# Optimization experiments

Measured on AMD Instinct MI355X. Metric: run time of the kernel, lower is better.

The kernel has to match this reference:

```python
import jax, jax.numpy as jnp
import numpy as np

N_NODES = 100000
N_EDGES = 3200000
N_GRAPHS = 64
IN_DIM = 4
HID = 64
EPS = 1e-5  # BatchNorm eps


def _batchnorm(x, gamma, beta):
    # training-mode batch norm over the node/graph axis (biased variance)
    mu = x.mean(axis=0)
    var = x.var(axis=0)
    return (x - mu) * jax.lax.rsqrt(var + EPS) * gamma + beta


def _gcn_conv(x, W, b, src, dst, n):
    # PyG GCNConv with add_self_loops=True, edge_weight=1:
    # out = D^{-1/2}(A+I)D^{-1/2} x W + b
    h = x @ W  # [N, out]
    deg = jax.ops.segment_sum(jnp.ones((src.shape[0],), h.dtype), dst,
                              num_segments=n) + 1.0  # +1 for self-loop
    dinv = jax.lax.rsqrt(deg)
    norm = dinv[src] * dinv[dst]  # [E]
    agg = jax.ops.segment_sum(h[src] * norm[:, None], dst, num_segments=n)
    # self-loop contribution: norm = 1/deg[i]
    return agg + h * (1.0 / deg)[:, None] + b


def setup_inputs() -> dict:
    key = jax.random.key(0)
    ks = jax.random.split(key, 12)
    s = 0.1
    inp = {
        "x": jax.random.normal(ks[0], (N_NODES, IN_DIM), jnp.float32),
        "edge_index": jax.random.randint(ks[1], (2, N_EDGES), 0, N_NODES, dtype=jnp.int64),
        "batch": jnp.sort(jax.random.randint(ks[2], (N_NODES,), 0, N_GRAPHS, dtype=jnp.int64)),
        # BatchNorm(4)
        "bn0_g": jnp.ones((IN_DIM,), jnp.float32),
        "bn0_b": jnp.zeros((IN_DIM,), jnp.float32),
        # GCNConv(4, 64)
        "W0": jax.random.normal(ks[3], (IN_DIM, HID), jnp.float32) * s,
        "b0": jnp.zeros((HID,), jnp.float32),
        # GCNConv(64, 64)
        "W1": jax.random.normal(ks[4], (HID, HID), jnp.float32) * s,
        "b1": jnp.zeros((HID,), jnp.float32),
        # BatchNorm(64) after pooling
        "bn1_g": jnp.ones((HID,), jnp.float32),
        "bn1_b": jnp.zeros((HID,), jnp.float32),
        # two hidden Linear(64, 64)
        "lin0_W": jax.random.normal(ks[5], (HID, HID), jnp.float32) * s,
        "lin0_b": jnp.zeros((HID,), jnp.float32),
        "lin1_W": jax.random.normal(ks[6], (HID, HID), jnp.float32) * s,
        "lin1_b": jnp.zeros((HID,), jnp.float32),
        # Linear(64, 1)
        "out_W": jax.random.normal(ks[7], (HID, 1), jnp.float32) * s,
        "out_b": jnp.zeros((1,), jnp.float32),
    }
    return inp


def reference(x, edge_index, batch, bn0_g, bn0_b, W0, b0, W1, b1,
              bn1_g, bn1_b, lin0_W, lin0_b, lin1_W, lin1_b, out_W, out_b):
    src, dst = edge_index[0], edge_index[1]
    h = _batchnorm(x, bn0_g, bn0_b)
    h = _gcn_conv(h, W0, b0, src, dst, N_NODES)
    h = _gcn_conv(h, W1, b1, src, dst, N_NODES)
    g = jax.ops.segment_sum(h, batch, num_segments=N_GRAPHS)  # global_add_pool
    g = _batchnorm(g, bn1_g, bn1_b)
    g = g @ lin0_W + lin0_b
    g = g @ lin1_W + lin1_b
    return g @ out_W + out_b  # [N_GRAPHS, 1]
```

## Files before the change

kernel.cpp:

```cpp
#include <hip/hip_runtime.h>
#include <hip/hip_bf16.h>

#define EPSF 1e-5f

static constexpr int NGRAPH = 64;
static constexpr int HBA = 512;
static constexpr int SH = 9;
static constexpr int GB = 256;
static constexpr int NBLK = 512;
static constexpr int BNB = 64;

__global__ __launch_bounds__(256) void k_pre(const float4* __restrict__ x,
                                             int N, const int* __restrict__ ei,
                                             int E, int chunk,
                                             float* __restrict__ bnpart,
                                             unsigned* __restrict__ counts) {
  __shared__ unsigned cnt[256];
  __shared__ float red[4][8];
  int t = threadIdx.x;
  if (blockIdx.x < BNB) {
    float s[4] = {0, 0, 0, 0}, q[4] = {0, 0, 0, 0};
    for (int i = blockIdx.x * 256 + t; i < N; i += BNB * 256) {
      float4 v = x[i];
      s[0] += v.x; q[0] += v.x * v.x;
      s[1] += v.y; q[1] += v.y * v.y;
      s[2] += v.z; q[2] += v.z * v.z;
      s[3] += v.w; q[3] += v.w * v.w;
    }
#pragma unroll
    for (int o = 32; o > 0; o >>= 1) {
#pragma unroll
      for (int k = 0; k < 4; k++) {
        s[k] += __shfl_down(s[k], o);
        q[k] += __shfl_down(q[k], o);
      }
    }
    int w = t >> 6;
    if ((t & 63) == 0) {
#pragma unroll
      for (int k = 0; k < 4; k++) {
        red[w][k] = s[k];
        red[w][4 + k] = q[k];
      }
    }
    __syncthreads();
    if (t < 8) {
      float a = red[0][t] + red[1][t] + red[2][t] + red[3][t];
      bnpart[blockIdx.x * 8 + t] = a;
    }
  } else {
    int g = blockIdx.x - BNB;
    cnt[t] = 0;
    __syncthreads();
    int lo = g * chunk, hi = min(E, lo + chunk);
    for (int base = lo + 4 * t; base < hi; base += 4 * 256) {
      int nv = min(4, hi - base);
      int d[4];
#pragma unroll
      for (int j = 0; j < 4; j++) d[j] = (j < nv) ? ei[E + base + j] : 0;
#pragma unroll
      for (int j = 0; j < 4; j++)
        if (j < nv) atomicAdd(&cnt[d[j] >> SH], 1u);
    }
    __syncthreads();
    counts[(size_t)g * 256 + t] = cnt[t];
  }
}

__global__ __launch_bounds__(1024) void k_boffA(
    const unsigned* __restrict__ counts, int E,
    const float* __restrict__ bnpart, unsigned* __restrict__ bucketStart,
    float* __restrict__ stats) {
  __shared__ unsigned tot4[1024];
  __shared__ unsigned tot[256];
  __shared__ unsigned scn[256];
  int tid = threadIdx.x;
  int b = tid & 255, q = tid >> 8;
  unsigned s = 0;
#pragma unroll 8
  for (int i = 0; i < 64; i++) s += counts[(size_t)(q * 64 + i) * 256 + b];
  tot4[tid] = s;
  if (tid < 8) {
    float a = 0.f;
#pragma unroll 8
    for (int i = 0; i < BNB; i++) a += bnpart[i * 8 + tid];
    stats[tid] = a;
  }
  __syncthreads();
  if (tid < 256) {
    unsigned v = tot4[tid] + tot4[256 + tid] + tot4[512 + tid] + tot4[768 + tid];
    tot[tid] = v;
    scn[tid] = v;
  }
  __syncthreads();
  for (int o = 1; o < 256; o <<= 1) {
    unsigned add = (tid < 256 && tid >= o) ? scn[tid - o] : 0u;
    __syncthreads();
    if (tid < 256) scn[tid] += add;
    __syncthreads();
  }
  if (tid < 256) bucketStart[tid] = scn[tid] - tot[tid];
  if (tid == 0) bucketStart[256] = (unsigned)E;
}

__global__ __launch_bounds__(256) void k_bases(
    const unsigned* __restrict__ counts,
    const unsigned* __restrict__ bucketStart, unsigned* __restrict__ bases) {
  __shared__ unsigned sc[256];
  __shared__ unsigned val[256];
  int b = blockIdx.x, g = threadIdx.x;
  unsigned c = counts[(size_t)g * 256 + b];
  val[g] = c;
  sc[g] = c;
  __syncthreads();
  for (int o = 1; o < 256; o <<= 1) {
    unsigned add = (g >= o) ? sc[g - o] : 0u;
    __syncthreads();
    sc[g] += add;
    __syncthreads();
  }
  bases[(size_t)g * 256 + b] = bucketStart[b] + sc[g] - val[g];
}

__global__ void k_bscatter(const int* __restrict__ ei, int E, int chunk,
                           const unsigned* __restrict__ bases,
                           unsigned* __restrict__ bedges) {
  __shared__ unsigned cursor[256];
  int g = blockIdx.x;
  if (threadIdx.x < 256)
    cursor[threadIdx.x] = bases[(size_t)g * 256 + threadIdx.x];
  __syncthreads();
  int lo = g * chunk, hi = min(E, lo + chunk);
  for (int base = lo + 4 * (int)threadIdx.x; base < hi;
       base += 4 * (int)blockDim.x) {
    int nv = min(4, hi - base);
    int s[4], d[4];
#pragma unroll
    for (int j = 0; j < 4; j++) {
      s[j] = (j < nv) ? ei[base + j] : 0;
      d[j] = (j < nv) ? ei[E + base + j] : 0;
    }
    unsigned pos[4];
#pragma unroll
    for (int j = 0; j < 4; j++)
      if (j < nv) pos[j] = atomicAdd(&cursor[d[j] >> SH], 1u);
#pragma unroll
    for (int j = 0; j < 4; j++)
      if (j < nv)
        bedges[pos[j]] = ((unsigned)s[j] << SH) | (unsigned)(d[j] & (HBA - 1));
  }
}

__device__ __forceinline__ void bn0_coefs(const float* __restrict__ stats,
                                          const float* __restrict__ g,
                                          const float* __restrict__ b,
                                          float Ninv, float* sc, float* sh) {
#pragma unroll
  for (int k = 0; k < 4; k++) {
    float mu = stats[k] * Ninv;
    float var = stats[4 + k] * Ninv - mu * mu;
    var = var < 0.f ? 0.f : var;
    float s = g[k] / sqrtf(var + EPSF);
    sc[k] = s;
    sh[k] = b[k] - mu * s;
  }
}

__global__ __launch_bounds__(512) void k_build(
    const unsigned* __restrict__ bedges,
    const unsigned* __restrict__ bucketStart, const float4* __restrict__ x,
    int N, const float* __restrict__ stats, const float* __restrict__ bn0g,
    const float* __restrict__ bn0b, float Ninv, unsigned* __restrict__ csrOff,
    uint4* __restrict__ pk, unsigned* __restrict__ csr) {
  __shared__ unsigned h[HBA];
  __shared__ unsigned scn[HBA];
  __shared__ unsigned cur[HBA];
  int t = threadIdx.x;
  int r = blockIdx.x;
  h[t] = 0;
  __syncthreads();
  int blo = bucketStart[r], bhi = bucketStart[r + 1];
  for (int base = blo + 4 * t; base < bhi; base += 4 * 512) {
    int nv = min(4, bhi - base);
    unsigned p[4];
#pragma unroll
    for (int j = 0; j < 4; j++) p[j] = (j < nv) ? bedges[base + j] : 0;
#pragma unroll
    for (int j = 0; j < 4; j++)
      if (j < nv) atomicAdd(&h[p[j] & (HBA - 1)], 1u);
  }
  __syncthreads();
  unsigned deg = h[t];
  scn[t] = deg;
  __syncthreads();
  for (int o = 1; o < HBA; o <<= 1) {
    unsigned add = (t >= o) ? scn[t - o] : 0u;
    __syncthreads();
    scn[t] += add;
    __syncthreads();
  }
  unsigned nodeOff = blo + scn[t] - deg;
  int v = (r << SH) + t;
  csrOff[v] = nodeOff;
  if (t == HBA - 1) csrOff[(r << SH) + HBA] = blo + scn[t];
  cur[t] = nodeOff;
  if (v < N) {
    float sco[4], sho[4];
    bn0_coefs(stats, bn0g, bn0b, Ninv, sco, sho);
    float dv = rsqrtf((float)deg + 1.0f);
    float4 xv = x[v];
    float zx = dv * (xv.x * sco[0] + sho[0]);
    float zy = dv * (xv.y * sco[1] + sho[1]);
    float zz = dv * (xv.z * sco[2] + sho[2]);
    float zw = dv * (xv.w * sco[3] + sho[3]);
    uint4 u;
    u.x = (__float_as_uint(zx) & ~15u) | (deg & 15u);
    u.y = (__float_as_uint(zy) & ~15u) | ((deg >> 4) & 15u);
    u.z = (__float_as_uint(zz) & ~15u) | ((deg >> 8) & 15u);
    u.w = (__float_as_uint(zw) & ~15u) | ((deg >> 12) & 15u);
    pk[v] = u;
  }
  __syncthreads();
  for (int base = blo + 4 * t; base < bhi; base += 4 * 512) {
    int nv = min(4, bhi - base);
    unsigned p[4];
#pragma unroll
    for (int j = 0; j < 4; j++) p[j] = (j < nv) ? bedges[base + j] : 0;
    unsigned pos[4];
#pragma unroll
    for (int j = 0; j < 4; j++)
      if (j < nv) pos[j] = atomicAdd(&cur[p[j] & (HBA - 1)], 1u);
#pragma unroll
    for (int j = 0; j < 4; j++)
      if (j < nv) csr[pos[j]] = p[j] >> SH;
  }
}

__global__ __launch_bounds__(256) void k_acc1f(
    const unsigned* __restrict__ csr, const unsigned* __restrict__ csrOff,
    const uint4* __restrict__ pk, const int* __restrict__ batch, int N,
    float4* __restrict__ p2, float* __restrict__ part1) {
  __shared__ float lac[NGRAPH * 6];
  for (int i = threadIdx.x; i < NGRAPH * 6; i += blockDim.x) lac[i] = 0.f;
  __syncthreads();
  int total = gridDim.x * blockDim.x;
  int iters = (N + total - 1) / total;
  int v = blockIdx.x * blockDim.x + threadIdx.x;
  for (int it = 0; it < iters; ++it, v += total) {
    bool act = v < N;
    float u0 = 0, u1 = 0, u2 = 0, u3 = 0, sv = 0, cv = 0;
    int g = 0;
    if (act) {
      unsigned o0 = csrOff[v], o1 = csrOff[v + 1];
      float a0 = 0, a1 = 0, a2 = 0, a3 = 0, asd = 0;
      for (unsigned e = o0; e < o1; e += 8) {
        int m = (int)min(8u, o1 - e);
        unsigned s[8];
        uint4 q[8];
#pragma unroll
        for (int j = 0; j < 8; j++) s[j] = (j < m) ? csr[e + j] : 0u;
#pragma unroll
        for (int j = 0; j < 8; j++)
          if (j < m) q[j] = pk[s[j]];
#pragma unroll
        for (int j = 0; j < 8; j++)
          if (j < m) {
            unsigned dg = (q[j].x & 15u) | ((q[j].y & 15u) << 4) |
                          ((q[j].z & 15u) << 8) | ((q[j].w & 15u) << 12);
            asd += rsqrtf((float)dg + 1.0f);
            a0 += __uint_as_float(q[j].x);
            a1 += __uint_as_float(q[j].y);
            a2 += __uint_as_float(q[j].z);
            a3 += __uint_as_float(q[j].w);
          }
      }
      unsigned deg = o1 - o0;
      float dv = rsqrtf((float)deg + 1.0f);
      float idg = dv * dv;
      uint4 qv = pk[v];
      float px = idg * (a0 + __uint_as_float(qv.x));
      float py = idg * (a1 + __uint_as_float(qv.y));
      float pz = idg * (a2 + __uint_as_float(qv.z));
      float pw = idg * (a3 + __uint_as_float(qv.w));
      p2[v] = make_float4(px, py, pz, pw);
      g = batch[v];
      u0 = dv * px; u1 = dv * py; u2 = dv * pz; u3 = dv * pw;
      sv = idg + dv * asd;
      cv = 1.0f;
    }
    if (__all(!act)) continue;
    int gf = __shfl(g, 0);
    bool uni = __all((!act) || (g == gf));
    if (uni) {
#pragma unroll
      for (int o = 32; o > 0; o >>= 1) {
        u0 += __shfl_down(u0, o);
        u1 += __shfl_down(u1, o);
        u2 += __shfl_down(u2, o);
        u3 += __shfl_down(u3, o);
        sv += __shfl_down(sv, o);
        cv += __shfl_down(cv, o);
      }
      if ((threadIdx.x & 63) == 0) {
        int g6 = gf * 6;
        atomicAdd(&lac[g6 + 0], u0);
        atomicAdd(&lac[g6 + 1], u1);
        atomicAdd(&lac[g6 + 2], u2);
        atomicAdd(&lac[g6 + 3], u3);
        atomicAdd(&lac[g6 + 4], sv);
        atomicAdd(&lac[g6 + 5], cv);
      }
    } else if (act) {
      int g6 = g * 6;
      atomicAdd(&lac[g6 + 0], u0);
      atomicAdd(&lac[g6 + 1], u1);
      atomicAdd(&lac[g6 + 2], u2);
      atomicAdd(&lac[g6 + 3], u3);
      atomicAdd(&lac[g6 + 4], sv);
      atomicAdd(&lac[g6 + 5], cv);
    }
  }
  __syncthreads();
  float* out = part1 + (size_t)blockIdx.x * (NGRAPH * 6);
  for (int i = threadIdx.x; i < NGRAPH * 6; i += blockDim.x) out[i] = lac[i];
}

__global__ __launch_bounds__(256) void k_acc2f(
    const unsigned* __restrict__ csr, const unsigned* __restrict__ csrOff,
    const float4* __restrict__ p2, const int* __restrict__ batch, int N,
    float* __restrict__ part2) {
  __shared__ float lac[NGRAPH * 4];
  for (int i = threadIdx.x; i < NGRAPH * 4; i += blockDim.x) lac[i] = 0.f;
  __syncthreads();
  int total = gridDim.x * blockDim.x;
  int iters = (N + total - 1) / total;
  int v = blockIdx.x * blockDim.x + threadIdx.x;
  for (int it = 0; it < iters; ++it, v += total) {
    bool act = v < N;
    float u0 = 0, u1 = 0, u2 = 0, u3 = 0;
    int g = 0;
    if (act) {
      unsigned o0 = csrOff[v], o1 = csrOff[v + 1];
      float t0 = 0, t1 = 0, t2 = 0, t3 = 0;
      for (unsigned e = o0; e < o1; e += 8) {
        int m = (int)min(8u, o1 - e);
        unsigned s[8];
        float4 q[8];
#pragma unroll
        for (int j = 0; j < 8; j++) s[j] = (j < m) ? csr[e + j] : 0u;
#pragma unroll
        for (int j = 0; j < 8; j++)
          if (j < m) q[j] = p2[s[j]];
#pragma unroll
        for (int j = 0; j < 8; j++)
          if (j < m) {
            t0 += q[j].x; t1 += q[j].y; t2 += q[j].z; t3 += q[j].w;
          }
      }
      float dv = rsqrtf((float)(o1 - o0) + 1.0f);
      g = batch[v];
      u0 = dv * t0; u1 = dv * t1; u2 = dv * t2; u3 = dv * t3;
    }
    if (__all(!act)) continue;
    int gf = __shfl(g, 0);
    bool uni = __all((!act) || (g == gf));
    if (uni) {
#pragma unroll
      for (int o = 32; o > 0; o >>= 1) {
        u0 += __shfl_down(u0, o);
        u1 += __shfl_down(u1, o);
        u2 += __shfl_down(u2, o);
        u3 += __shfl_down(u3, o);
      }
      if ((threadIdx.x & 63) == 0) {
        int g4 = gf * 4;
        atomicAdd(&lac[g4 + 0], u0);
        atomicAdd(&lac[g4 + 1], u1);
        atomicAdd(&lac[g4 + 2], u2);
        atomicAdd(&lac[g4 + 3], u3);
      }
    } else if (act) {
      int g4 = g * 4;
      atomicAdd(&lac[g4 + 0], u0);
      atomicAdd(&lac[g4 + 1], u1);
      atomicAdd(&lac[g4 + 2], u2);
      atomicAdd(&lac[g4 + 3], u3);
    }
  }
  __syncthreads();
  float* out = part2 + (size_t)blockIdx.x * (NGRAPH * 4);
  for (int i = threadIdx.x; i < NGRAPH * 4; i += blockDim.x) out[i] = lac[i];
}

__global__ __launch_bounds__(1024) void k_final(
    const float* __restrict__ part1, const float* __restrict__ part2,
    const float* __restrict__ W0, const float* __restrict__ b0,
    const float* __restrict__ W1, const float* __restrict__ b1,
    const float* __restrict__ bn1g, const float* __restrict__ bn1b,
    const float* __restrict__ l0W, const float* __restrict__ l0b,
    const float* __restrict__ l1W, const float* __restrict__ l1b,
    const float* __restrict__ oW, const float* __restrict__ ob,
    float* __restrict__ out) {
  __shared__ float sP1[NGRAPH * 6];
  __shared__ float sU2[NGRAPH * 4];
  __shared__ float sW01[4 * 64];
  __shared__ float sb01[64];
  __shared__ float sA[4096];
  __shared__ float sB[4096];
  __shared__ float sSc[64], sSh[64];
  __shared__ float wW1[4096], wl0[4096], wl1[4096];
  int t = threadIdx.x;
  for (int i = t; i < 4096; i += 1024) {
    wW1[i] = W1[i];
    wl0[i] = l0W[i];
    wl1[i] = l1W[i];
  }
  if (t < NGRAPH * 6) {
    float s = 0.f;
#pragma unroll 8
    for (int b = 0; b < NBLK; b++) s += part1[(size_t)b * (NGRAPH * 6) + t];
    sP1[t] = s;
  } else if (t < NGRAPH * 6 + NGRAPH * 4) {
    int i = t - NGRAPH * 6;
    float s = 0.f;
#pragma unroll 8
    for (int b = 0; b < NBLK; b++) s += part2[(size_t)b * (NGRAPH * 4) + i];
    sU2[i] = s;
  }
  __syncthreads();
  if (t < 256) {
    int k = t >> 6, f = t & 63;
    float a = 0.f;
#pragma unroll
    for (int j = 0; j < 64; j++) a += W0[k * 64 + j] * wW1[j * 64 + f];
    sW01[t] = a;
  } else if (t < 320) {
    int f = t - 256;
    float a = 0.f;
#pragma unroll
    for (int j = 0; j < 64; j++) a += b0[j] * wW1[j * 64 + f];
    sb01[f] = a;
  }
  __syncthreads();
  for (int idx = t; idx < 4096; idx += 1024) {
    int G = idx >> 6, f = idx & 63;
    float v = sP1[G * 6 + 5] * b1[f] + sP1[G * 6 + 4] * sb01[f];
    v += (sU2[G * 4 + 0] + sP1[G * 6 + 0]) * sW01[0 * 64 + f];
    v += (sU2[G * 4 + 1] + sP1[G * 6 + 1]) * sW01[1 * 64 + f];
    v += (sU2[G * 4 + 2] + sP1[G * 6 + 2]) * sW01[2 * 64 + f];
    v += (sU2[G * 4 + 3] + sP1[G * 6 + 3]) * sW01[3 * 64 + f];
    sA[idx] = v;
  }
  __syncthreads();
  if (t < 64) {
    float mu = 0.f;
#pragma unroll
    for (int G = 0; G < 64; G++) mu += sA[G * 64 + t];
    mu *= (1.0f / 64.0f);
    float var = 0.f;
#pragma unroll
    for (int G = 0; G < 64; G++) {
      float d = sA[G * 64 + t] - mu;
      var += d * d;
    }
    var *= (1.0f / 64.0f);
    float s = bn1g[t] / sqrtf(var + EPSF);
    sSc[t] = s;
    sSh[t] = bn1b[t] - mu * s;
  }
  __syncthreads();
  for (int idx = t; idx < 4096; idx += 1024) {
    int f = idx & 63;
    sA[idx] = sA[idx] * sSc[f] + sSh[f];
  }
  __syncthreads();
  for (int idx = t; idx < 4096; idx += 1024) {
    int G = idx >> 6, f = idx & 63;
    float v = l0b[f];
#pragma unroll
    for (int j = 0; j < 64; j++) v += sA[G * 64 + j] * wl0[j * 64 + f];
    sB[idx] = v;
  }
  __syncthreads();
  for (int idx = t; idx < 4096; idx += 1024) {
    int G = idx >> 6, f = idx & 63;
    float v = l1b[f];
#pragma unroll
    for (int j = 0; j < 64; j++) v += sB[G * 64 + j] * wl1[j * 64 + f];
    sA[idx] = v;
  }
  __syncthreads();
  if (t < 64) {
    float v = ob[0];
#pragma unroll
    for (int j = 0; j < 64; j++) v += sA[t * 64 + j] * oW[j];
    out[t] = v;
  }
}

extern "C" void kernel_launch(void* const* d_in, const int* in_sizes, int n_in,
                              void* d_out, int out_size, void* d_ws,
                              size_t ws_size, hipStream_t stream) {
  const float* x = (const float*)d_in[0];
  const int* ei = (const int*)d_in[1];
  const int* batch = (const int*)d_in[2];
  const float* bn0g = (const float*)d_in[3];
  const float* bn0b = (const float*)d_in[4];
  const float* W0 = (const float*)d_in[5];
  const float* b0 = (const float*)d_in[6];
  const float* W1 = (const float*)d_in[7];
  const float* b1 = (const float*)d_in[8];
  const float* bn1g = (const float*)d_in[9];
  const float* bn1b = (const float*)d_in[10];
  const float* l0W = (const float*)d_in[11];
  const float* l0b = (const float*)d_in[12];
  const float* l1W = (const float*)d_in[13];
  const float* l1b = (const float*)d_in[14];
  const float* oW = (const float*)d_in[15];
  const float* ob = (const float*)d_in[16];

  const int N = in_sizes[0] / 4;
  const int E = in_sizes[1] / 2;
  const int RA = (N + HBA - 1) >> SH;
  const int chunk = (E + GB - 1) / GB;

  size_t off = 0;
  auto alloc = [&](size_t nbytes) {
    size_t cur = (off + 63) & ~(size_t)63;
    off = cur + nbytes;
    return (void*)((char*)d_ws + cur);
  };
  float* stats = (float*)alloc(8 * 4);
  float* bnpart = (float*)alloc((size_t)BNB * 8 * 4);
  unsigned* bucketStart = (unsigned*)alloc((size_t)(256 + 1) * 4);
  float* part1 = (float*)alloc((size_t)NBLK * NGRAPH * 6 * 4);
  float* part2 = (float*)alloc((size_t)NBLK * NGRAPH * 4 * 4);
  unsigned* csrOff = (unsigned*)alloc(((size_t)RA * HBA + 1) * 4);
  uint4* pk = (uint4*)alloc((size_t)N * 16);
  unsigned* bedges = (unsigned*)alloc((size_t)E * 4);
  size_t arena_bytes = (size_t)E * 4;
  char* arena = (char*)alloc(arena_bytes);
  unsigned* counts = (unsigned*)arena;
  unsigned* bases = (unsigned*)(arena + (size_t)256 * GB * 4);
  unsigned* csr = (unsigned*)arena;
  float4* p2 = (float4*)bedges;
  (void)ws_size;

  const float Ninv = 1.0f / (float)N;
  k_pre<<<BNB + GB, 256, 0, stream>>>((const float4*)x, N, ei, E, chunk,
                                      bnpart, counts);
  k_boffA<<<1, 1024, 0, stream>>>(counts, E, bnpart, bucketStart, stats);
  k_bases<<<256, 256, 0, stream>>>(counts, bucketStart, bases);
  k_bscatter<<<GB, 256, 0, stream>>>(ei, E, chunk, bases, bedges);
  k_build<<<RA, 512, 0, stream>>>(bedges, bucketStart, (const float4*)x, N,
                                  stats, bn0g, bn0b, Ninv, csrOff, pk, csr);
  k_acc1f<<<NBLK, 256, 0, stream>>>(csr, csrOff, pk, batch, N, p2, part1);
  k_acc2f<<<NBLK, 256, 0, stream>>>(csr, csrOff, p2, batch, N, part2);
  k_final<<<1, 1024, 0, stream>>>(part1, part2, W0, b0, W1, b1, bn1g, bn1b,
                                  l0W, l0b, l1W, l1b, oW, ob, (float*)d_out);
}
```

Baseline: 260.1 us.

## Pad CSR rows to multiples of four and pack degree into p2 for vector index loads

Each node's CSR row is padded to a multiple of four entries, with a per-bucket slack, so the accumulation kernels can read neighbour indices as 16-byte uint4 loads instead of scalar loads. Degree is now recovered from the low bits packed into pk and p2, so csrOff[v+1] is no longer read. This saves index load instructions and one offset read per node. It costs extra padding writes, a larger arena, and slight precision loss in p2 because its low mantissa bits now hold the degree.

```diff
diff --git a/kernel.cpp b/kernel.cpp
--- a/kernel.cpp
+++ b/kernel.cpp
@@ -191,7 +191,8 @@
   }
   __syncthreads();
   unsigned deg = h[t];
-  scn[t] = deg;
+  unsigned degP = (deg + 3u) & ~3u;
+  scn[t] = degP;
   __syncthreads();
   for (int o = 1; o < HBA; o <<= 1) {
     unsigned add = (t >= o) ? scn[t - o] : 0u;
@@ -199,10 +200,10 @@
     scn[t] += add;
     __syncthreads();
   }
-  unsigned nodeOff = blo + scn[t] - deg;
+  unsigned csrBase = (((unsigned)blo + 3u) & ~3u) + 2304u * (unsigned)r;
+  unsigned nodeOff = csrBase + scn[t] - degP;
   int v = (r << SH) + t;
   csrOff[v] = nodeOff;
-  if (t == HBA - 1) csrOff[(r << SH) + HBA] = blo + scn[t];
   cur[t] = nodeOff;
   if (v < N) {
     float sco[4], sho[4];
@@ -234,12 +235,13 @@
     for (int j = 0; j < 4; j++)
       if (j < nv) csr[pos[j]] = p[j] >> SH;
   }
+  for (unsigned i = deg; i < degP; i++) csr[nodeOff + i] = 0u;
 }
 
 __global__ __launch_bounds__(256) void k_acc1f(
     const unsigned* __restrict__ csr, const unsigned* __restrict__ csrOff,
     const uint4* __restrict__ pk, const int* __restrict__ batch, int N,
-    float4* __restrict__ p2, float* __restrict__ part1) {
+    uint4* __restrict__ p2, float* __restrict__ part1) {
   __shared__ float lac[NGRAPH * 6];
   for (int i = threadIdx.x; i < NGRAPH * 6; i += blockDim.x) lac[i] = 0.f;
   __syncthreads();
@@ -251,14 +253,19 @@
     float u0 = 0, u1 = 0, u2 = 0, u3 = 0, sv = 0, cv = 0;
     int g = 0;
     if (act) {
-      unsigned o0 = csrOff[v], o1 = csrOff[v + 1];
+      uint4 qv = pk[v];
+      unsigned deg = (qv.x & 15u) | ((qv.y & 15u) << 4) |
+                     ((qv.z & 15u) << 8) | ((qv.w & 15u) << 12);
+      unsigned degP = (deg + 3u) & ~3u;
+      unsigned o0 = csrOff[v];
+      const uint4* cp = (const uint4*)(csr + o0);
       float a0 = 0, a1 = 0, a2 = 0, a3 = 0, asd = 0;
-      for (unsigned e = o0; e < o1; e += 8) {
-        int m = (int)min(8u, o1 - e);
-        unsigned s[8];
+      for (unsigned e = 0; e < degP; e += 8) {
+        uint4 i0 = cp[e >> 2];
+        uint4 i1 = cp[(e >> 2) + 1];
+        unsigned s[8] = {i0.x, i0.y, i0.z, i0.w, i1.x, i1.y, i1.z, i1.w};
+        int m = (int)(deg - e);
         uint4 q[8];
-#pragma unroll
-        for (int j = 0; j < 8; j++) s[j] = (j < m) ? csr[e + j] : 0u;
 #pragma unroll
         for (int j = 0; j < 8; j++)
           if (j < m) q[j] = pk[s[j]];
@@ -274,17 +281,23 @@
             a3 += __uint_as_float(q[j].w);
           }
       }
-      unsigned deg = o1 - o0;
       float dv = rsqrtf((float)deg + 1.0f);
       float idg = dv * dv;
-      uint4 qv = pk[v];
       float px = idg * (a0 + __uint_as_float(qv.x));
       float py = idg * (a1 + __uint_as_float(qv.y));
       float pz = idg * (a2 + __uint_as_float(qv.z));
       float pw = idg * (a3 + __uint_as_float(qv.w));
-      p2[v] = make_float4(px, py, pz, pw);
+      uint4 o;
+      o.x = (__float_as_uint(px) & ~15u) | (deg & 15u);
+      o.y = (__float_as_uint(py) & ~15u) | ((deg >> 4) & 15u);
+      o.z = (__float_as_uint(pz) & ~15u) | ((deg >> 8) & 15u);
+      o.w = (__float_as_uint(pw) & ~15u) | ((deg >> 12) & 15u);
+      p2[v] = o;
       g = batch[v];
-      u0 = dv * px; u1 = dv * py; u2 = dv * pz; u3 = dv * pw;
+      u0 = dv * __uint_as_float(o.x);
+      u1 = dv * __uint_as_float(o.y);
+      u2 = dv * __uint_as_float(o.z);
+      u3 = dv * __uint_as_float(o.w);
       sv = idg + dv * asd;
       cv = 1.0f;
     }
@@ -327,7 +340,7 @@
 
 __global__ __launch_bounds__(256) void k_acc2f(
     const unsigned* __restrict__ csr, const unsigned* __restrict__ csrOff,
-    const float4* __restrict__ p2, const int* __restrict__ batch, int N,
+    const uint4* __restrict__ p2, const int* __restrict__ batch, int N,
     float* __restrict__ part2) {
   __shared__ float lac[NGRAPH * 4];
   for (int i = threadIdx.x; i < NGRAPH * 4; i += blockDim.x) lac[i] = 0.f;
@@ -340,24 +353,32 @@
     float u0 = 0, u1 = 0, u2 = 0, u3 = 0;
     int g = 0;
     if (act) {
-      unsigned o0 = csrOff[v], o1 = csrOff[v + 1];
+      uint4 pv = p2[v];
+      unsigned deg = (pv.x & 15u) | ((pv.y & 15u) << 4) |
+                     ((pv.z & 15u) << 8) | ((pv.w & 15u) << 12);
+      unsigned degP = (deg + 3u) & ~3u;
+      unsigned o0 = csrOff[v];
+      const uint4* cp = (const uint4*)(csr + o0);
       float t0 = 0, t1 = 0, t2 = 0, t3 = 0;
-      for (unsigned e = o0; e < o1; e += 8) {
-        int m = (int)min(8u, o1 - e);
-        unsigned s[8];
-        float4 q[8];
-#pragma unroll
-        for (int j = 0; j < 8; j++) s[j] = (j < m) ? csr[e + j] : 0u;
+      for (unsigned e = 0; e < degP; e += 8) {
+        uint4 i0 = cp[e >> 2];
+        uint4 i1 = cp[(e >> 2) + 1];
+        unsigned s[8] = {i0.x, i0.y, i0.z, i0.w, i1.x, i1.y, i1.z, i1.w};
+        int m = (int)(deg - e);
+        uint4 q[8];
 #pragma unroll
         for (int j = 0; j < 8; j++)
           if (j < m) q[j] = p2[s[j]];
 #pragma unroll
         for (int j = 0; j < 8; j++)
           if (j < m) {
-            t0 += q[j].x; t1 += q[j].y; t2 += q[j].z; t3 += q[j].w;
+            t0 += __uint_as_float(q[j].x);
+            t1 += __uint_as_float(q[j].y);
+            t2 += __uint_as_float(q[j].z);
+            t3 += __uint_as_float(q[j].w);
           }
       }
-      float dv = rsqrtf((float)(o1 - o0) + 1.0f);
+      float dv = rsqrtf((float)deg + 1.0f);
       g = batch[v];
       u0 = dv * t0; u1 = dv * t1; u2 = dv * t2; u3 = dv * t3;
     }
@@ -538,12 +559,12 @@
   unsigned* csrOff = (unsigned*)alloc(((size_t)RA * HBA + 1) * 4);
   uint4* pk = (uint4*)alloc((size_t)N * 16);
   unsigned* bedges = (unsigned*)alloc((size_t)E * 4);
-  size_t arena_bytes = (size_t)E * 4;
+  size_t arena_bytes = ((size_t)E + 2304 * (size_t)RA + 4096) * 4;
   char* arena = (char*)alloc(arena_bytes);
   unsigned* counts = (unsigned*)arena;
   unsigned* bases = (unsigned*)(arena + (size_t)256 * GB * 4);
   unsigned* csr = (unsigned*)arena;
-  float4* p2 = (float4*)bedges;
+  uint4* p2 = (uint4*)bedges;
   (void)ws_size;
 
   const float Ninv = 1.0f / (float)N;
```

After: 255.0 us. Within noise of the previous version (-2.0%).
